# Optimization experiments

Hardware: AMD Instinct MI355X
Metric: run time of the kernel (lower is better)

Reference implementation:

```python
import jax, jax.numpy as jnp
from jax import lax
import numpy as np

B, CTX, TGT, D_MODEL = 2, 1024, 256, 512
EXPAND, D_STATE, D_CONV, N_LAYERS = 2, 16, 4, 2
D_INNER = EXPAND * D_MODEL
DT_RANK = (D_MODEL + 15) // 16  # 32, mamba_ssm default ceil(d_model/16)
LN_EPS = 1e-5


def setup_inputs() -> dict:
    key = jax.random.key(0)
    ks = jax.random.split(key, 20)
    s = 0.02
    inp = {
        "context_repr": jax.random.normal(ks[0], (B, CTX, D_MODEL), jnp.float32),
        "target_time_emb": jax.random.normal(ks[1], (B, TGT, D_MODEL), jnp.float32),
        "target_var_emb": jax.random.normal(ks[2], (B, TGT, D_MODEL), jnp.float32),
        "target_count": TGT,
        # position_proj / output_proj / LayerNorm params
        "pos_w": jax.random.normal(ks[3], (D_MODEL, 2 * D_MODEL), jnp.float32) * s,
        "pos_b": jnp.zeros((D_MODEL,), jnp.float32),
        "outp_w": jax.random.normal(ks[4], (D_MODEL, D_MODEL), jnp.float32) * s,
        "outp_b": jnp.zeros((D_MODEL,), jnp.float32),
        "ln_g": jnp.ones((D_MODEL,), jnp.float32),
        "ln_b": jnp.zeros((D_MODEL,), jnp.float32),
        # stacked per-layer Mamba params
        "in_w": jax.random.normal(ks[5], (N_LAYERS, 2 * D_INNER, D_MODEL), jnp.float32) * s,
        "conv_w": jax.random.normal(ks[6], (N_LAYERS, D_INNER, D_CONV), jnp.float32) * s,
        "conv_b": jnp.zeros((N_LAYERS, D_INNER), jnp.float32),
        "xproj_w": jax.random.normal(ks[7], (N_LAYERS, DT_RANK + 2 * D_STATE, D_INNER), jnp.float32) * s,
        "dt_w": jax.random.normal(ks[8], (N_LAYERS, D_INNER, DT_RANK), jnp.float32) * s,
        "dt_b": jax.random.normal(ks[9], (N_LAYERS, D_INNER), jnp.float32) * s,
        # A_log init as in mamba_ssm: A = arange(1, d_state+1) repeated over d_inner
        "A_log": jnp.broadcast_to(
            jnp.log(jnp.arange(1, D_STATE + 1, dtype=jnp.float32)),
            (N_LAYERS, D_INNER, D_STATE),
        ).copy(),
        "D_skip": jnp.ones((N_LAYERS, D_INNER), jnp.float32),
        "out_w": jax.random.normal(ks[10], (N_LAYERS, D_MODEL, D_INNER), jnp.float32) * s,
    }
    return inp


def _mamba_block(x, in_w, conv_w, conv_b, xproj_w, dt_w, dt_b, A_log, D_skip, out_w):
    # x: [B, L, d_model]
    Bb, L, _ = x.shape
    xz = jnp.einsum("bld,ed->ble", x, in_w)          # [B, L, 2*d_inner]
    xc, z = jnp.split(xz, 2, axis=-1)
    # causal depthwise conv1d (Conv1d pad=d_conv-1 then [..., :L])
    xt = xc.transpose(0, 2, 1)                        # [B, d_inner, L]
    conv = lax.conv_general_dilated(
        xt, conv_w[:, None, :], (1,), [(D_CONV - 1, 0)],
        feature_group_count=D_INNER,
        dimension_numbers=("NCH", "OIH", "NCH"),
    )
    u = jax.nn.silu(conv + conv_b[None, :, None]).transpose(0, 2, 1)  # [B, L, d_inner]
    x_dbl = jnp.einsum("bld,ed->ble", u, xproj_w)     # [B, L, dt_rank + 2*d_state]
    dt, Bm, Cm = jnp.split(x_dbl, [DT_RANK, DT_RANK + D_STATE], axis=-1)
    delta = jax.nn.softplus(jnp.einsum("blr,dr->bld", dt, dt_w) + dt_b)  # [B, L, d_inner]
    A = -jnp.exp(A_log)                               # [d_inner, d_state]
    dA = jnp.exp(delta[..., None] * A)                # [B, L, d_inner, d_state]
    dBu = delta[..., None] * Bm[:, :, None, :] * u[..., None]

    def step(h, inps):
        dA_t, dBu_t, C_t = inps                       # [B,d_inner,d_state], same, [B,d_state]
        h = dA_t * h + dBu_t
        y = jnp.einsum("bds,bs->bd", h, C_t)
        return h, y

    h0 = jnp.zeros((Bb, D_INNER, D_STATE), x.dtype)
    _, ys = lax.scan(step, h0, (dA.transpose(1, 0, 2, 3), dBu.transpose(1, 0, 2, 3), Cm.transpose(1, 0, 2)))
    y = ys.transpose(1, 0, 2) + u * D_skip            # [B, L, d_inner]
    y = y * jax.nn.silu(z)
    return jnp.einsum("ble,de->bld", y, out_w)        # [B, L, d_model]


def reference(context_repr, target_time_emb, target_var_emb, target_count,
              pos_w, pos_b, outp_w, outp_b, ln_g, ln_b,
              in_w, conv_w, conv_b, xproj_w, dt_w, dt_b, A_log, D_skip, out_w):
    tc = jnp.concatenate([target_time_emb, target_var_emb], axis=-1)      # [B, T, 2*d]
    pos = jnp.einsum("blk,dk->bld", tc, pos_w) + pos_b                    # [B, T, d]
    x = jnp.concatenate([context_repr, pos], axis=1)                      # [B, C+T, d]
    for i in range(N_LAYERS):
        x = x + _mamba_block(x, in_w[i], conv_w[i], conv_b[i], xproj_w[i],
                             dt_w[i], dt_b[i], A_log[i], D_skip[i], out_w[i])
    mu = jnp.mean(x, axis=-1, keepdims=True)
    var = jnp.mean(jnp.square(x - mu), axis=-1, keepdims=True)
    x = (x - mu) * lax.rsqrt(var + LN_EPS) * ln_g + ln_b
    tgt = x[:, -int(target_count):]
    return jnp.einsum("bld,ed->ble", tgt, outp_w) + outp_b
```

## Files before the change

### kernel.cpp

```cpp
#include <hip/hip_runtime.h>
#include <hip/hip_bf16.h>

#define B_     2
#define CTX_   1024
#define TGT_   256
#define DM_    512
#define L_     1280
#define DI_    1024
#define DS_    16
#define DCONV_ 4
#define NL_    2
#define DTR_   32
#define MROWS_ (B_*L_)
#define NC_    80
#define CL_    16
#define XDBL_N_ (MROWS_*64)

typedef unsigned short u16;
typedef __attribute__((ext_vector_type(8))) __bf16 bf16x8;
typedef __attribute__((ext_vector_type(4))) float f32x4;

__device__ __forceinline__ float sigmoidf_(float v){ return 1.f/(1.f+__expf(-v)); }
__device__ __forceinline__ float siluf_(float v){ return v*sigmoidf_(v); }
__device__ __forceinline__ float softplusf_(float v){ return (v>20.f)?v:log1pf(__expf(v)); }
__device__ __forceinline__ u16 f2b(float f){
    union { float f; unsigned u; } x; x.f = f;
    unsigned u = x.u;
    return (u16)((u + 0x7fffu + ((u>>16)&1u)) >> 16);
}
__device__ __forceinline__ float b2f(u16 v){ return __uint_as_float(((unsigned)v)<<16); }
__device__ __forceinline__ void gload_lds16(const void* g, void* l){
    __builtin_amdgcn_global_load_lds((const __attribute__((address_space(1))) unsigned*)g,
                                     (__attribute__((address_space(3))) unsigned*)l, 16, 0, 0);
}
#define PIPE_SYNC do{ asm volatile("s_waitcnt vmcnt(0)" ::: "memory"); \
                      __builtin_amdgcn_sched_barrier(0); \
                      __builtin_amdgcn_s_barrier(); \
                      __builtin_amdgcn_sched_barrier(0); }while(0)

#define XCD_SWZ(bx, by) \
    int nwg_ = gridDim.x*gridDim.y; \
    int id_  = blockIdx.y*gridDim.x + blockIdx.x; \
    int swz_ = (id_ & 7)*(nwg_>>3) + (id_>>3); \
    int bx = swz_ % gridDim.x, by = swz_ / gridDim.x;

#define G0_ 262144
#define G1_ 131072
#define G2_  65536
#define G3_  32768
#define G4_  16384
__global__ __launch_bounds__(256) void k_init(const float* __restrict__ s0, const float* __restrict__ s1,
                                              const float* __restrict__ s2, const float* __restrict__ s3,
                                              const float* __restrict__ s4,
                                              u16* d0, u16* d1, u16* d2, u16* d3, u16* d4,
                                              const float* __restrict__ ctx, const float* __restrict__ te,
                                              const float* __restrict__ ve, float* __restrict__ x,
                                              u16* __restrict__ xb, u16* __restrict__ tcb,
                                              float* __restrict__ xdbl0, float* __restrict__ xdbl1){
    int blk = blockIdx.x;
    if (blk < 1984){
        int g = blk*256 + threadIdx.x;
        const float* s; u16* d; int base;
        if      (g < G0_)                { s=s0; d=d0; base=g*8; }
        else if (g < G0_+G1_)            { s=s1; d=d1; base=(g-G0_)*8; }
        else if (g < G0_+G1_+G2_)        { s=s2; d=d2; base=(g-G0_-G1_)*8; }
        else if (g < G0_+G1_+G2_+G3_)    { s=s3; d=d3; base=(g-G0_-G1_-G2_)*8; }
        else                             { s=s4; d=d4; base=(g-G0_-G1_-G2_-G3_)*8; }
        float4 a = *(const float4*)&s[base];
        float4 b = *(const float4*)&s[base+4];
        union { u16 us[8]; uint4 v; } o;
        o.us[0]=f2b(a.x); o.us[1]=f2b(a.y); o.us[2]=f2b(a.z); o.us[3]=f2b(a.w);
        o.us[4]=f2b(b.x); o.us[5]=f2b(b.y); o.us[6]=f2b(b.z); o.us[7]=f2b(b.w);
        *(uint4*)&d[base] = o.v;
    } else if (blk < 1984+1024){
        int e = ((blk-1984)*256 + threadIdx.x)*4;
        int d = e % DM_;
        int l = (e/DM_) % CTX_;
        int b = e/(DM_*CTX_);
        float4 v = *(const float4*)&ctx[e];
        size_t o = ((size_t)(b*L_+l))*DM_ + d;
        *(float4*)&x[o] = v;
        union { u16 us[4]; uint2 q; } p;
        p.us[0]=f2b(v.x); p.us[1]=f2b(v.y); p.us[2]=f2b(v.z); p.us[3]=f2b(v.w);
        *(uint2*)&xb[o] = p.q;
    } else if (blk < 1984+1024+512){
        int e = ((blk-1984-1024)*256 + threadIdx.x)*4;
        int k = e % (2*DM_);
        int r = e / (2*DM_);
        float4 v = (k < DM_) ? *(const float4*)&te[(size_t)r*DM_ + k]
                             : *(const float4*)&ve[(size_t)r*DM_ + (k-DM_)];
        union { u16 us[4]; uint2 q; } p;
        p.us[0]=f2b(v.x); p.us[1]=f2b(v.y); p.us[2]=f2b(v.z); p.us[3]=f2b(v.w);
        *(uint2*)&tcb[e] = p.q;
    } else if (blk < 3520+160){
        int j = ((blk-3520)*256 + threadIdx.x)*4;
        *(float4*)&xdbl0[j] = make_float4(0.f,0.f,0.f,0.f);
    } else {
        int j = ((blk-3680)*256 + threadIdx.x)*4;
        *(float4*)&xdbl1[j] = make_float4(0.f,0.f,0.f,0.f);
    }
}

template<bool WB>
__global__ __launch_bounds__(512) void k_mmx(const u16* __restrict__ A, int lda,
                                             const u16* __restrict__ Bw, int ldb,
                                             float* __restrict__ C, int ldc,
                                             const float* __restrict__ bias, int K,
                                             u16* __restrict__ Cb, int ldcb){
    __shared__ u16 As[2][128*64];
    __shared__ u16 Bs[2][128*64];
    int tid = threadIdx.x;
    int wave = tid >> 6, lane = tid & 63;
    XCD_SWZ(bx, by);
    int bm = by*128, bn = bx*128;
    int wr = (wave>>2)*64, wc = (wave&3)*32;
    f32x4 acc[4][2] = {};
    int lrow = lane & 15, lk = (lane>>4)*8;
    int dphys0 = tid*16;
    int dphys1 = dphys0 + 8192;
    int alog0  = dphys0 ^ (((dphys0>>7)&7)<<4);
    int alog1  = dphys1 ^ (((dphys1>>7)&7)<<4);
    int grow0  = alog0 >> 7,         grow1 = alog1 >> 7;
    int gcol0  = (alog0 & 127) >> 1, gcol1 = (alog1 & 127) >> 1;
    const u16* Ar0 = A  + (size_t)(bm+grow0)*lda + gcol0;
    const u16* Ar1 = A  + (size_t)(bm+grow1)*lda + gcol1;
    const u16* Br0 = Bw + (size_t)(bn+grow0)*ldb + gcol0;
    const u16* Br1 = Bw + (size_t)(bn+grow1)*ldb + gcol1;
    int aoff[4][2], boff[2][2];
    #pragma unroll
    for (int f=0; f<4; ++f){
        int ra = wr + f*16 + lrow;
        #pragma unroll
        for (int s=0;s<2;++s) aoff[f][s] = (ra*128 + s*64 + lk*2) ^ ((ra&7)<<4);
    }
    #pragma unroll
    for (int f=0; f<2; ++f){
        int rb = wc + f*16 + lrow;
        #pragma unroll
        for (int s=0;s<2;++s) boff[f][s] = (rb*128 + s*64 + lk*2) ^ ((rb&7)<<4);
    }
    int nt = K >> 6;
    auto stage = [&](int t, int buf){
        int k0 = t*64;
        gload_lds16(Ar0 + k0, &As[buf][wave*512]);
        gload_lds16(Ar1 + k0, &As[buf][4096 + wave*512]);
        gload_lds16(Br0 + k0, &Bs[buf][wave*512]);
        gload_lds16(Br1 + k0, &Bs[buf][4096 + wave*512]);
    };
    stage(0, 0);
    PIPE_SYNC;
    int cur = 0;
    for (int t=0; t<nt; ++t){
        if (t+1 < nt) stage(t+1, cur^1);
        #pragma unroll
        for (int s=0;s<2;++s){
            bf16x8 af[4], bfr[2];
            #pragma unroll
            for (int f=0; f<4; ++f) af[f]  = *(const bf16x8*)((const char*)As[cur] + aoff[f][s]);
            #pragma unroll
            for (int f=0; f<2; ++f) bfr[f] = *(const bf16x8*)((const char*)Bs[cur] + boff[f][s]);
            #pragma unroll
            for (int fm=0; fm<4; ++fm)
                #pragma unroll
                for (int fn=0; fn<2; ++fn)
                    acc[fm][fn] = __builtin_amdgcn_mfma_f32_16x16x32_bf16(af[fm], bfr[fn], acc[fm][fn], 0,0,0);
        }
        PIPE_SYNC;
        cur ^= 1;
    }
    #pragma unroll
    for (int fm=0; fm<4; ++fm){
        int m0 = bm + wr + fm*16 + (lane>>4)*4;
        #pragma unroll
        for (int fn=0; fn<2; ++fn){
            int n = bn + wc + fn*16 + (lane&15);
            float bsv = (!WB && bias) ? bias[n] : 0.f;
            #pragma unroll
            for (int j=0; j<4; ++j){
                float v = acc[fm][fn][j] + bsv;
                if (WB) Cb[(size_t)(m0+j)*ldcb + n] = f2b(v);
                else    C [(size_t)(m0+j)*ldc  + n] = v;
            }
        }
    }
}

template<bool ACC, bool SCAT>
__global__ __launch_bounds__(512) void k_mmx64(const u16* __restrict__ A, int lda,
                                               const u16* __restrict__ Bw, int ldb,
                                               float* __restrict__ C, int ldc,
                                               const float* __restrict__ bias, int ksteps,
                                               u16* __restrict__ Cb, int ldcb){
    __shared__ u16 As[2][64*128];
    __shared__ u16 Bs[2][64*128];
    int tid = threadIdx.x;
    int wave = tid >> 6, lane = tid & 63;
    XCD_SWZ(bx, by);
    int bm = by*64;
    int bn = bx*64;
    int wr = (wave>>2)*32, wc = (wave&3)*16;
    f32x4 acc[2] = {};
    int lrow = lane & 15, lk = (lane>>4)*8;
    int w4 = wave & 3;
    bool isB = wave >= 4;
    const u16* Base = isB ? Bw : A;
    int ldS  = isB ? ldb : lda;
    int brow = isB ? bn : bm;
    const u16* Sr[4];
    int dstoff[4];
    #pragma unroll
    for (int i=0;i<4;++i){
        int dphys = i*4096 + w4*1024 + lane*16;
        int alog  = dphys ^ (((dphys>>8)&7)<<4);
        int grow  = alog >> 8;
        int gcol  = (alog & 255) >> 1;
        Sr[i] = Base + (size_t)(brow+grow)*ldS + gcol;
        dstoff[i] = i*2048 + w4*512;
    }
    int aoff[2][4], boff4[4];
    #pragma unroll
    for (int f=0; f<2; ++f){
        int ra = wr + f*16 + lrow;
        #pragma unroll
        for (int s=0;s<4;++s) aoff[f][s] = (ra*256 + s*64 + lk*2) ^ ((ra&7)<<4);
    }
    { int rb = wc + lrow;
      #pragma unroll
      for (int s=0;s<4;++s) boff4[s] = (rb*256 + s*64 + lk*2) ^ ((rb&7)<<4); }
    auto stage = [&](int t, int buf){
        int k0 = t*128;
        u16* dstbuf = isB ? &Bs[buf][0] : &As[buf][0];
        #pragma unroll
        for (int i=0;i<4;++i) gload_lds16(Sr[i] + k0, dstbuf + dstoff[i]);
    };
    stage(0, 0);
    PIPE_SYNC;
    int cur = 0;
    for (int t = 0; t < ksteps; ++t){
        if (t+1 < ksteps) stage(t+1, cur^1);
        #pragma unroll
        for (int s=0;s<4;++s){
            bf16x8 af[2], bfr;
            #pragma unroll
            for (int f=0; f<2; ++f) af[f] = *(const bf16x8*)((const char*)As[cur] + aoff[f][s]);
            bfr = *(const bf16x8*)((const char*)Bs[cur] + boff4[s]);
            #pragma unroll
            for (int fm=0; fm<2; ++fm)
                acc[fm] = __builtin_amdgcn_mfma_f32_16x16x32_bf16(af[fm], bfr, acc[fm], 0,0,0);
        }
        PIPE_SYNC;
        cur ^= 1;
    }
    #pragma unroll
    for (int fm=0; fm<2; ++fm){
        int m0 = bm + wr + fm*16 + (lane>>4)*4;
        int n = bn + wc + (lane&15);
        float bsv = bias ? bias[n] : 0.f;
        #pragma unroll
        for (int j=0; j<4; ++j){
            float v = acc[fm][j] + bsv;
            int m = m0 + j;
            if (SCAT){
                int xrow = (m>>8)*L_ + CTX_ + (m&255);
                C [(size_t)xrow*ldc  + n] = v;
                Cb[(size_t)xrow*ldcb + n] = f2b(v);
            } else {
                size_t off = (size_t)m*ldc + n;
                if (ACC) v += C[off];
                C[off] = v;
                if (Cb) Cb[(size_t)m*ldcb + n] = f2b(v);
            }
        }
    }
}

__global__ __launch_bounds__(512) void k_xproj(const u16* __restrict__ xzb, const u16* __restrict__ Bw,
                                               float* __restrict__ C, const float* __restrict__ cw,
                                               const float* __restrict__ cb){
    __shared__ u16 As[64*32];
    __shared__ u16 Bs[64*32];
    __shared__ u16 sXC[67*32];
    int tid = threadIdx.x;
    int wave = tid >> 6, lane = tid & 63;
    XCD_SWZ(bx, by);
    int bm = by*64;
    int kbase = bx*128;
    int b0row = (bm/L_)*L_;
    int wr = (wave>>2)*32, wc = (wave&3)*16;
    f32x4 acc[2] = {};
    int lrow = lane & 15, lk = (lane>>4)*8;
    int w4 = wave & 3;
    int dphys = w4*1024 + lane*16;
    int alog  = dphys ^ (((dphys>>7)&7)<<4);
    int grow  = alog >> 6;
    int gcol  = (alog & 63) >> 1;
    const u16* Br = Bw + (size_t)grow*DI_ + gcol;
    int aoff[2], boff;
    #pragma unroll
    for (int f=0; f<2; ++f){
        int ra = wr + f*16 + lrow;
        aoff[f] = (ra*64 + lk*2) ^ (((ra>>1)&7)<<4);
    }
    { int rb = wc + lrow; boff = (rb*64 + lk*2) ^ (((rb>>1)&7)<<4); }
    for (int t = 0; t < 4; ++t){
        int k0 = kbase + t*32;
        if (wave >= 4) gload_lds16(Br + k0, &Bs[w4*512]);
        if (tid < 268){
            int rr = tid >> 2, c16 = (tid & 3)*8;
            int gr = bm + rr - 3;
            uint4 v = make_uint4(0,0,0,0);
            if (gr >= b0row) v = *(const uint4*)&xzb[(size_t)gr*2048 + k0 + c16];
            *(uint4*)&sXC[rr*32 + c16] = v;
        }
        __syncthreads();
        {
            int o = tid*4, rr = o >> 5, cc0 = o & 31;
            union { u16 us[4]; uint2 q; } w;
            #pragma unroll
            for (int j=0;j<4;++j){
                int cc = cc0 + j, d = k0 + cc;
                float4 wv = *(const float4*)&cw[d*4];
                float a = cb[d];
                a = fmaf(b2f(sXC[(rr+0)*32+cc]), wv.x, a);
                a = fmaf(b2f(sXC[(rr+1)*32+cc]), wv.y, a);
                a = fmaf(b2f(sXC[(rr+2)*32+cc]), wv.z, a);
                a = fmaf(b2f(sXC[(rr+3)*32+cc]), wv.w, a);
                w.us[j] = f2b(siluf_(a));
            }
            int L0 = rr*64 + cc0*2;
            int ph = L0 ^ (((L0>>7)&7)<<4);
            *(uint2*)((char*)As + ph) = w.q;
        }
        __syncthreads();
        bf16x8 af[2], bfr;
        #pragma unroll
        for (int f=0; f<2; ++f) af[f] = *(const bf16x8*)((const char*)As + aoff[f]);
        bfr = *(const bf16x8*)((const char*)Bs + boff);
        #pragma unroll
        for (int fm=0; fm<2; ++fm)
            acc[fm] = __builtin_amdgcn_mfma_f32_16x16x32_bf16(af[fm], bfr, acc[fm], 0,0,0);
        __syncthreads();
    }
    #pragma unroll
    for (int fm=0; fm<2; ++fm){
        int m0 = bm + wr + fm*16 + (lane>>4)*4;
        int n = wc + (lane&15);
        #pragma unroll
        for (int j=0; j<4; ++j)
            atomicAdd(&C[(size_t)(m0+j)*64 + n], acc[fm][j]);
    }
}

__global__ __launch_bounds__(256) void k_scan1(const u16* __restrict__ xzb, const float* __restrict__ xdbl,
                                               const float* __restrict__ dtw, const float* __restrict__ dtb,
                                               const float* __restrict__ cw, const float* __restrict__ cb,
                                               const float* __restrict__ Alog,
                                               u16* __restrict__ hend, u16* __restrict__ P){
    __shared__ float sX[CL_*64];
    __shared__ float sW[64*33];
    __shared__ float sDtb[64];
    __shared__ float sDel[CL_*64];
    __shared__ float sU[CL_*64];
    __shared__ u16   sXC[19*64];
    int blk = blockIdx.x;
    int dgrp = blk & 15;
    int c = (blk>>4) % NC_;
    int b = blk/(16*NC_);
    int d0 = dgrp*64;
    int tid = threadIdx.x;
    size_t rowbase = (size_t)(b*L_ + c*CL_);
    {
        int e = tid*4;
        *(float4*)&sX[e] = *(const float4*)&xdbl[rowbase*64 + e];
        int w0 = tid*8, dr = w0>>5, kk = w0&31;
        float4 wa = *(const float4*)&dtw[(size_t)(d0+dr)*DTR_ + kk];
        float4 wb = *(const float4*)&dtw[(size_t)(d0+dr)*DTR_ + kk + 4];
        sW[dr*33+kk+0]=wa.x; sW[dr*33+kk+1]=wa.y; sW[dr*33+kk+2]=wa.z; sW[dr*33+kk+3]=wa.w;
        sW[dr*33+kk+4]=wb.x; sW[dr*33+kk+5]=wb.y; sW[dr*33+kk+6]=wb.z; sW[dr*33+kk+7]=wb.w;
        if (tid < 64) sDtb[tid] = dtb[d0+tid];
    }
    if (tid < 152){
        int rr = tid >> 3, c8 = (tid & 7)*8;
        long gr = (long)rowbase + rr - 3;
        uint4 v = make_uint4(0,0,0,0);
        if (gr >= (long)b*L_) v = *(const uint4*)&xzb[(size_t)gr*2048 + d0 + c8];
        *(uint4*)&sXC[rr*64 + c8] = v;
    }
    __syncthreads();
    {
        int o = tid*4, t = o>>6, dd0 = o&63;
        #pragma unroll
        for (int j=0;j<4;++j){
            int dd = dd0 + j, d = d0 + dd;
            float4 wv = *(const float4*)&cw[d*4];
            float a = cb[d];
            a = fmaf(b2f(sXC[(t+0)*64+dd]), wv.x, a);
            a = fmaf(b2f(sXC[(t+1)*64+dd]), wv.y, a);
            a = fmaf(b2f(sXC[(t+2)*64+dd]), wv.z, a);
            a = fmaf(b2f(sXC[(t+3)*64+dd]), wv.w, a);
            sU[t*64+dd] = siluf_(a);
        }
    }
    #pragma unroll
    for (int i=0;i<4;++i){
        int idx = tid + i*256;
        int t = idx>>6, dd = idx&63;
        float acc = sDtb[dd];
        #pragma unroll
        for (int k=0;k<DTR_;++k) acc = fmaf(sX[t*64+k], sW[dd*33+k], acc);
        sDel[idx] = softplusf_(acc);
    }
    __syncthreads();
    int dl = tid>>2, sg = (tid&3)*4;
    int d = d0 + dl;
    float A[4];
    #pragma unroll
    for (int i=0;i<4;++i) A[i] = -__expf(Alog[d*DS_ + sg + i]);
    float h[4] = {0,0,0,0}, Pl[4] = {1.f,1.f,1.f,1.f};
    #pragma unroll
    for (int t=0;t<CL_;++t){
        float delta = sDel[t*64+dl];
        float du    = delta*sU[t*64+dl];
        #pragma unroll
        for (int i=0;i<4;++i){
            float a = __expf(delta*A[i]);
            h[i]  = fmaf(a, h[i], du*sX[t*64 + 32 + sg + i]);
            Pl[i] *= a;
        }
    }
    size_t ob = ((size_t)((b*NC_+c)*DI_) + d)*DS_ + sg;
    union { u16 us[4]; uint2 q; } oh, op;
    #pragma unroll
    for (int i=0;i<4;++i){ oh.us[i]=f2b(h[i]); op.us[i]=f2b(Pl[i]); }
    *(uint2*)&hend[ob] = oh.q;
    *(uint2*)&P[ob]    = op.q;
}

__global__ __launch_bounds__(256) void k_scan2(u16* __restrict__ hend, const u16* __restrict__ P){
    int g = blockIdx.x*256 + threadIdx.x;
    int s = g & 15;
    int d = (g>>4) & 1023;
    int b = g>>14;
    size_t base = ((size_t)b*NC_*DI_ + d)*DS_ + s;
    const size_t cs = (size_t)DI_*DS_;
    float h = 0.f;
    for (int c0=0;c0<NC_;c0+=8){
        float he[8], p[8];
        #pragma unroll
        for (int j=0;j<8;++j){ size_t idx = base + (size_t)(c0+j)*cs; he[j]=b2f(hend[idx]); p[j]=b2f(P[idx]); }
        #pragma unroll
        for (int j=0;j<8;++j){ size_t idx = base + (size_t)(c0+j)*cs; hend[idx]=f2b(h); h=fmaf(p[j],h,he[j]); }
    }
}

__global__ __launch_bounds__(256) void k_scan3(const u16* __restrict__ xzb, const float* __restrict__ xdbl,
                                               const float* __restrict__ dtw, const float* __restrict__ dtb,
                                               const float* __restrict__ cw, const float* __restrict__ cb,
                                               const float* __restrict__ Alog, const float* __restrict__ Dsk,
                                               const u16* __restrict__ hstart, u16* __restrict__ yb){
    __shared__ float sX[CL_*64];
    __shared__ float sW[64*33];
    __shared__ float sDtb[64];
    __shared__ float sDel[CL_*64];
    __shared__ float sU[CL_*64];
    __shared__ float sY[CL_*64];
    __shared__ u16   sXC[19*64];
    int blk = blockIdx.x;
    int dgrp = blk & 15;
    int c = (blk>>4) % NC_;
    int b = blk/(16*NC_);
    int d0 = dgrp*64;
    int tid = threadIdx.x;
    size_t rowbase = (size_t)(b*L_ + c*CL_);
    {
        int e = tid*4;
        *(float4*)&sX[e] = *(const float4*)&xdbl[rowbase*64 + e];
        int w0 = tid*8, dr = w0>>5, kk = w0&31;
        float4 wa = *(const float4*)&dtw[(size_t)(d0+dr)*DTR_ + kk];
        float4 wb = *(const float4*)&dtw[(size_t)(d0+dr)*DTR_ + kk + 4];
        sW[dr*33+kk+0]=wa.x; sW[dr*33+kk+1]=wa.y; sW[dr*33+kk+2]=wa.z; sW[dr*33+kk+3]=wa.w;
        sW[dr*33+kk+4]=wb.x; sW[dr*33+kk+5]=wb.y; sW[dr*33+kk+6]=wb.z; sW[dr*33+kk+7]=wb.w;
        if (tid < 64) sDtb[tid] = dtb[d0+tid];
    }
    if (tid < 152){
        int rr = tid >> 3, c8 = (tid & 7)*8;
        long gr = (long)rowbase + rr - 3;
        uint4 v = make_uint4(0,0,0,0);
        if (gr >= (long)b*L_) v = *(const uint4*)&xzb[(size_t)gr*2048 + d0 + c8];
        *(uint4*)&sXC[rr*64 + c8] = v;
    }
    __syncthreads();
    {
        int o = tid*4, t = o>>6, dd0 = o&63;
        #pragma unroll
        for (int j=0;j<4;++j){
            int dd = dd0 + j, d = d0 + dd;
            float4 wv = *(const float4*)&cw[d*4];
            float a = cb[d];
            a = fmaf(b2f(sXC[(t+0)*64+dd]), wv.x, a);
            a = fmaf(b2f(sXC[(t+1)*64+dd]), wv.y, a);
            a = fmaf(b2f(sXC[(t+2)*64+dd]), wv.z, a);
            a = fmaf(b2f(sXC[(t+3)*64+dd]), wv.w, a);
            sU[t*64+dd] = siluf_(a);
        }
    }
    #pragma unroll
    for (int i=0;i<4;++i){
        int idx = tid + i*256;
        int t = idx>>6, dd = idx&63;
        float acc = sDtb[dd];
        #pragma unroll
        for (int k=0;k<DTR_;++k) acc = fmaf(sX[t*64+k], sW[dd*33+k], acc);
        sDel[idx] = softplusf_(acc);
    }
    __syncthreads();
    int dl = tid>>2, sg = (tid&3)*4;
    int d = d0 + dl;
    float A[4];
    #pragma unroll
    for (int i=0;i<4;++i) A[i] = -__expf(Alog[d*DS_ + sg + i]);
    size_t ib = ((size_t)((b*NC_+c)*DI_) + d)*DS_ + sg;
    uint2 hq = *(const uint2*)&hstart[ib];
    float h[4] = { b2f((u16)(hq.x&0xffffu)), b2f((u16)(hq.x>>16)),
                   b2f((u16)(hq.y&0xffffu)), b2f((u16)(hq.y>>16)) };
    #pragma unroll
    for (int t=0;t<CL_;++t){
        float delta = sDel[t*64+dl];
        float du    = delta*sU[t*64+dl];
        float yt = 0.f;
        #pragma unroll
        for (int i=0;i<4;++i){
            float a = __expf(delta*A[i]);
            h[i] = fmaf(a, h[i], du*sX[t*64 + 32 + sg + i]);
            yt   = fmaf(h[i], sX[t*64 + 48 + sg + i], yt);
        }
        yt += __shfl_xor(yt, 1);
        yt += __shfl_xor(yt, 2);
        if ((tid&3)==0) sY[t*64+dl] = yt;
    }
    __syncthreads();
    {
        int e = tid*4, st = e>>6, dd = e&63;
        size_t off = (rowbase+st)*DI_ + d0 + dd;
        float4 dskv = *(const float4*)&Dsk[d0+dd];
        uint2 zz = *(const uint2*)&xzb[(rowbase+st)*2048 + DI_ + d0 + dd];
        float z0 = __uint_as_float(zz.x<<16),  z1 = __uint_as_float(zz.x & 0xffff0000u);
        float z2 = __uint_as_float(zz.y<<16),  z3 = __uint_as_float(zz.y & 0xffff0000u);
        union { u16 us[4]; uint2 q; } o;
        o.us[0] = f2b((sY[e+0] + sU[e+0]*dskv.x) * siluf_(z0));
        o.us[1] = f2b((sY[e+1] + sU[e+1]*dskv.y) * siluf_(z1));
        o.us[2] = f2b((sY[e+2] + sU[e+2]*dskv.z) * siluf_(z2));
        o.us[3] = f2b((sY[e+3] + sU[e+3]*dskv.w) * siluf_(z3));
        *(uint2*)&yb[off] = o.q;
    }
}

__global__ __launch_bounds__(512) void k_lnmm(const float* __restrict__ x, const float* __restrict__ g_,
                                              const float* __restrict__ be_,
                                              const u16* __restrict__ Bw,
                                              const float* __restrict__ bias, float* __restrict__ out){
    __shared__ u16 ALn[64*512];
    __shared__ u16 Bs[2][64*128];
    int tid = threadIdx.x;
    int wave = tid >> 6, lane = tid & 63;
    int bm = blockIdx.y*64, bn = blockIdx.x*64;
    for (int rr8 = 0; rr8 < 8; ++rr8){
        int rr = wave*8 + rr8;
        int tr = bm + rr;
        int xrow = (tr>>8)*L_ + CTX_ + (tr&255);
        const float* row = x + (size_t)xrow*DM_ + lane*8;
        float4 a = *(const float4*)row;
        float4 b = *(const float4*)(row+4);
        float s  = a.x+a.y+a.z+a.w + b.x+b.y+b.z+b.w;
        float sq = a.x*a.x+a.y*a.y+a.z*a.z+a.w*a.w + b.x*b.x+b.y*b.y+b.z*b.z+b.w*b.w;
        #pragma unroll
        for (int off=32; off; off>>=1){ s += __shfl_xor(s,off); sq += __shfl_xor(sq,off); }
        float mu = s*(1.f/DM_);
        float rs = rsqrtf(sq*(1.f/DM_) - mu*mu + 1e-5f);
        int c0 = lane*8;
        float4 g0 = *(const float4*)&g_[c0],  g1 = *(const float4*)&g_[c0+4];
        float4 b0 = *(const float4*)&be_[c0], b1 = *(const float4*)&be_[c0+4];
        union { u16 us[8]; uint4 v; } o;
        o.us[0]=f2b((a.x-mu)*rs*g0.x+b0.x); o.us[1]=f2b((a.y-mu)*rs*g0.y+b0.y);
        o.us[2]=f2b((a.z-mu)*rs*g0.z+b0.z); o.us[3]=f2b((a.w-mu)*rs*g0.w+b0.w);
        o.us[4]=f2b((b.x-mu)*rs*g1.x+b1.x); o.us[5]=f2b((b.y-mu)*rs*g1.y+b1.y);
        o.us[6]=f2b((b.z-mu)*rs*g1.z+b1.z); o.us[7]=f2b((b.w-mu)*rs*g1.w+b1.w);
        int ph = (rr*1024) + ((lane*16) ^ ((rr&7)<<4));
        *(uint4*)((char*)ALn + ph) = o.v;
    }
    __syncthreads();
    int wr = (wave>>2)*32, wc = (wave&3)*16;
    f32x4 acc[2] = {};
    int lrow = lane & 15, lk = (lane>>4)*8;
    int w4 = wave & 3;
    const u16* Sr[4];
    int dstoff[4];
    #pragma unroll
    for (int i=0;i<4;++i){
        int dphys = i*4096 + w4*1024 + lane*16;
        int alog  = dphys ^ (((dphys>>8)&7)<<4);
        int grow  = alog >> 8;
        int gcol  = (alog & 255) >> 1;
        Sr[i] = Bw + (size_t)(bn+grow)*DM_ + gcol;
        dstoff[i] = i*2048 + w4*512;
    }
    int boff4[4];
    { int rb = wc + lrow;
      #pragma unroll
      for (int s=0;s<4;++s) boff4[s] = (rb*256 + s*64 + lk*2) ^ ((rb&7)<<4); }
    int ra0 = wr + lrow, ra1 = wr + 16 + lrow;
    auto stage = [&](int t, int buf){
        if (wave >= 4){
            int k0 = t*128;
            #pragma unroll
            for (int i=0;i<4;++i) gload_lds16(Sr[i] + k0, &Bs[buf][0] + dstoff[i]);
        }
    };
    stage(0, 0);
    PIPE_SYNC;
    int cur = 0;
    for (int t = 0; t < 4; ++t){
        if (t+1 < 4) stage(t+1, cur^1);
        #pragma unroll
        for (int s=0;s<4;++s){
            int kb = (t*128 + s*32 + lk)*2;
            bf16x8 af0 = *(const bf16x8*)((const char*)ALn + (ra0*1024 + (kb ^ ((ra0&7)<<4))));
            bf16x8 af1 = *(const bf16x8*)((const char*)ALn + (ra1*1024 + (kb ^ ((ra1&7)<<4))));
            bf16x8 bfr = *(const bf16x8*)((const char*)Bs[cur] + boff4[s]);
            acc[0] = __builtin_amdgcn_mfma_f32_16x16x32_bf16(af0, bfr, acc[0], 0,0,0);
            acc[1] = __builtin_amdgcn_mfma_f32_16x16x32_bf16(af1, bfr, acc[1], 0,0,0);
        }
        PIPE_SYNC;
        cur ^= 1;
    }
    #pragma unroll
    for (int fm=0; fm<2; ++fm){
        int m0 = bm + wr + fm*16 + (lane>>4)*4;
        int n = bn + wc + (lane&15);
        float bsv = bias[n];
        #pragma unroll
        for (int j=0; j<4; ++j)
            out[(size_t)(m0+j)*DM_ + n] = acc[fm][j] + bsv;
    }
}

extern "C" void kernel_launch(void* const* d_in, const int* in_sizes, int n_in,
                              void* d_out, int out_size, void* d_ws, size_t ws_size,
                              hipStream_t stream) {
    const float* ctx    = (const float*)d_in[0];
    const float* te     = (const float*)d_in[1];
    const float* ve     = (const float*)d_in[2];
    const float* pos_w  = (const float*)d_in[4];
    const float* pos_b  = (const float*)d_in[5];
    const float* outp_w = (const float*)d_in[6];
    const float* outp_b = (const float*)d_in[7];
    const float* ln_g   = (const float*)d_in[8];
    const float* ln_b   = (const float*)d_in[9];
    const float* in_w   = (const float*)d_in[10];
    const float* conv_w = (const float*)d_in[11];
    const float* conv_b = (const float*)d_in[12];
    const float* xproj_w= (const float*)d_in[13];
    const float* dt_w   = (const float*)d_in[14];
    const float* dt_b   = (const float*)d_in[15];
    const float* A_log  = (const float*)d_in[16];
    const float* D_skip = (const float*)d_in[17];
    const float* out_w  = (const float*)d_in[18];
    float* out = (float*)d_out;

    float* ws    = (float*)d_ws;
    float* x     = ws;
    float* xdbl0 = x     + 1310720;
    float* xdbl1 = xdbl0 + 163840;
    u16*  hend  = (u16*)(xdbl1 + 163840);
    u16*  P     = hend  + 2621440;
    u16*  xb    = P     + 2621440;
    u16*  tcb   = xb    + 1310720;
    u16*  yb    = tcb   + 524288;
    u16*  xzb   = yb    + 2621440;
    u16*  inwb  = xzb   + 5242880;
    u16*  outwb = inwb  + 2097152;
    u16*  poswb = outwb + 1048576;
    u16*  outpwb= poswb + 524288;
    u16*  xpwb  = outpwb+ 262144;

    k_init<<<3840, 256, 0, stream>>>(in_w, out_w, pos_w, outp_w, xproj_w,
                                     inwb, outwb, poswb, outpwb, xpwb,
                                     ctx, te, ve, x, xb, tcb, xdbl0, xdbl1);
    k_mmx64<false,true><<<dim3(8,8), 512, 0, stream>>>(tcb, 2*DM_, poswb, 2*DM_, x, DM_, pos_b, 8, xb, DM_);

    for (int i=0;i<NL_;++i){
        const u16*   inwbi  = inwb + (size_t)i*2*DI_*DM_;
        const float* cw     = conv_w  + (size_t)i*DI_*DCONV_;
        const float* cb     = conv_b  + (size_t)i*DI_;
        const u16*   xpwbi  = xpwb + (size_t)i*(DTR_+2*DS_)*DI_;
        const float* dtw    = dt_w    + (size_t)i*DI_*DTR_;
        const float* dtb    = dt_b    + (size_t)i*DI_;
        const float* Ai     = A_log   + (size_t)i*DI_*DS_;
        const float* Dsk    = D_skip  + (size_t)i*DI_;
        const u16*   outwbi = outwb + (size_t)i*DM_*DI_;
        float*       xdbl   = (i == 0) ? xdbl0 : xdbl1;

        k_mmx<true><<<dim3(16,20), 512, 0, stream>>>(xb, DM_, inwbi, DM_, nullptr, 0, nullptr, DM_, xzb, 2*DI_);
        k_xproj<<<dim3(8,40), 512, 0, stream>>>(xzb, xpwbi, xdbl, cw, cb);
        k_scan1<<<2560, 256, 0, stream>>>(xzb, xdbl, dtw, dtb, cw, cb, Ai, hend, P);
        k_scan2<<<128, 256, 0, stream>>>(hend, P);
        k_scan3<<<2560, 256, 0, stream>>>(xzb, xdbl, dtw, dtb, cw, cb, Ai, Dsk, hend, yb);
        k_mmx64<true,false><<<dim3(8,40), 512, 0, stream>>>(yb, DI_, outwbi, DI_, x, DM_, nullptr, 8, xb, DM_);
    }

    k_lnmm<<<dim3(8,8), 512, 0, stream>>>(x, ln_g, ln_b, outpwb, outp_b, out);
}
```

Baseline: 208.1 us.

## Fuse chunk-carry scan into scan1 via last-block atomic counter

Removes the separate k_scan2 launch. Each scan1 block bumps a per-(batch, channel-group) counter after writing its chunk state. The last of the 80 chunk blocks for that group then runs the sequential carry propagation over all chunks. This saves one kernel launch and its dependency gap per layer, at the cost of a threadfence plus atomic in every block. The tail work is also concentrated on 32 late blocks, each handling 1024 sequences with 4 per thread, so parallelism in the tail may drop.

```diff
diff --git a/kernel.cpp b/kernel.cpp
--- a/kernel.cpp
+++ b/kernel.cpp
@@ -56,7 +56,8 @@
                                               const float* __restrict__ ctx, const float* __restrict__ te,
                                               const float* __restrict__ ve, float* __restrict__ x,
                                               u16* __restrict__ xb, u16* __restrict__ tcb,
-                                              float* __restrict__ xdbl0, float* __restrict__ xdbl1){
+                                              float* __restrict__ xdbl0, float* __restrict__ xdbl1,
+                                              int* __restrict__ cnt){
     int blk = blockIdx.x;
     if (blk < 1984){
         int g = blk*256 + threadIdx.x;
@@ -95,9 +96,11 @@
     } else if (blk < 3520+160){
         int j = ((blk-3520)*256 + threadIdx.x)*4;
         *(float4*)&xdbl0[j] = make_float4(0.f,0.f,0.f,0.f);
-    } else {
+    } else if (blk < 3680+160){
         int j = ((blk-3680)*256 + threadIdx.x)*4;
         *(float4*)&xdbl1[j] = make_float4(0.f,0.f,0.f,0.f);
+    } else {
+        if (threadIdx.x < 32) cnt[threadIdx.x] = 0;
     }
 }
 
@@ -355,13 +358,15 @@
                                                const float* __restrict__ dtw, const float* __restrict__ dtb,
                                                const float* __restrict__ cw, const float* __restrict__ cb,
                                                const float* __restrict__ Alog,
-                                               u16* __restrict__ hend, u16* __restrict__ P){
+                                               u16* __restrict__ hend, u16* __restrict__ P,
+                                               int* __restrict__ cnt){
     __shared__ float sX[CL_*64];
     __shared__ float sW[64*33];
     __shared__ float sDtb[64];
     __shared__ float sDel[CL_*64];
     __shared__ float sU[CL_*64];
     __shared__ u16   sXC[19*64];
+    __shared__ int   lastFlag;
     int blk = blockIdx.x;
     int dgrp = blk & 15;
     int c = (blk>>4) % NC_;
@@ -434,22 +439,41 @@
     for (int i=0;i<4;++i){ oh.us[i]=f2b(h[i]); op.us[i]=f2b(Pl[i]); }
     *(uint2*)&hend[ob] = oh.q;
     *(uint2*)&P[ob]    = op.q;
-}
-
-__global__ __launch_bounds__(256) void k_scan2(u16* __restrict__ hend, const u16* __restrict__ P){
-    int g = blockIdx.x*256 + threadIdx.x;
-    int s = g & 15;
-    int d = (g>>4) & 1023;
-    int b = g>>14;
-    size_t base = ((size_t)b*NC_*DI_ + d)*DS_ + s;
-    const size_t cs = (size_t)DI_*DS_;
-    float h = 0.f;
-    for (int c0=0;c0<NC_;c0+=8){
-        float he[8], p[8];
-        #pragma unroll
-        for (int j=0;j<8;++j){ size_t idx = base + (size_t)(c0+j)*cs; he[j]=b2f(hend[idx]); p[j]=b2f(P[idx]); }
-        #pragma unroll
-        for (int j=0;j<8;++j){ size_t idx = base + (size_t)(c0+j)*cs; hend[idx]=f2b(h); h=fmaf(p[j],h,he[j]); }
+    __threadfence();
+    __syncthreads();
+    if (tid == 0){
+        int old = atomicAdd(&cnt[b*16 + dgrp], 1);
+        lastFlag = (old == NC_ - 1);
+    }
+    __syncthreads();
+    if (lastFlag){
+        __threadfence();
+        size_t bases[4];
+        float hh[4] = {0.f,0.f,0.f,0.f};
+        #pragma unroll
+        for (int j=0;j<4;++j){
+            int seq = tid + j*256;
+            bases[j] = ((size_t)(b*NC_)*DI_ + d0 + (seq>>4))*DS_ + (seq&15);
+        }
+        const size_t cs = (size_t)DI_*DS_;
+        for (int c0=0;c0<NC_;c0+=4){
+            float he[4][4], pp[4][4];
+            #pragma unroll
+            for (int j=0;j<4;++j)
+                #pragma unroll
+                for (int q=0;q<4;++q){
+                    size_t idx = bases[j] + (size_t)(c0+q)*cs;
+                    he[j][q]=b2f(hend[idx]); pp[j][q]=b2f(P[idx]);
+                }
+            #pragma unroll
+            for (int j=0;j<4;++j)
+                #pragma unroll
+                for (int q=0;q<4;++q){
+                    size_t idx = bases[j] + (size_t)(c0+q)*cs;
+                    hend[idx]=f2b(hh[j]); hh[j]=fmaf(pp[j][q],hh[j],he[j][q]);
+                }
+        }
+        if (tid == 0) cnt[b*16 + dgrp] = 0;
     }
 }
 
@@ -682,10 +706,11 @@
     u16*  poswb = outwb + 1048576;
     u16*  outpwb= poswb + 524288;
     u16*  xpwb  = outpwb+ 262144;
-
-    k_init<<<3840, 256, 0, stream>>>(in_w, out_w, pos_w, outp_w, xproj_w,
+    int*  cnt   = (int*)(xpwb + 131072);
+
+    k_init<<<3841, 256, 0, stream>>>(in_w, out_w, pos_w, outp_w, xproj_w,
                                      inwb, outwb, poswb, outpwb, xpwb,
-                                     ctx, te, ve, x, xb, tcb, xdbl0, xdbl1);
+                                     ctx, te, ve, x, xb, tcb, xdbl0, xdbl1, cnt);
     k_mmx64<false,true><<<dim3(8,8), 512, 0, stream>>>(tcb, 2*DM_, poswb, 2*DM_, x, DM_, pos_b, 8, xb, DM_);
 
     for (int i=0;i<NL_;++i){
@@ -702,8 +727,7 @@
 
         k_mmx<true><<<dim3(16,20), 512, 0, stream>>>(xb, DM_, inwbi, DM_, nullptr, 0, nullptr, DM_, xzb, 2*DI_);
         k_xproj<<<dim3(8,40), 512, 0, stream>>>(xzb, xpwbi, xdbl, cw, cb);
-        k_scan1<<<2560, 256, 0, stream>>>(xzb, xdbl, dtw, dtb, cw, cb, Ai, hend, P);
-        k_scan2<<<128, 256, 0, stream>>>(hend, P);
+        k_scan1<<<2560, 256, 0, stream>>>(xzb, xdbl, dtw, dtb, cw, cb, Ai, hend, P, cnt);
         k_scan3<<<2560, 256, 0, stream>>>(xzb, xdbl, dtw, dtb, cw, cb, Ai, Dsk, hend, yb);
         k_mmx64<true,false><<<dim3(8,40), 512, 0, stream>>>(yb, DI_, outwbi, DI_, x, DM_, nullptr, 8, xb, DM_);
     }
```

Result: slower. 698.9 us (+235.9%).
